# Kernel tuning notes

Measured on AMD Instinct MI355X. Metric: run time of the kernel, lower is better.

The kernel has to match this reference:

```python
import jax, jax.numpy as jnp
import numpy as np


def conv2d(x, w, b=None, stride=1, pad=0):
    y = jax.lax.conv_general_dilated(x, w, (stride, stride), [(pad, pad), (pad, pad)],
                                     dimension_numbers=('NCHW', 'OIHW', 'NCHW'))
    if b is not None:
        y = y + b[None, :, None, None]
    return y


def dcn_v2(x, off, mask, w, b):
    # ModulatedDeformConv, k=3, stride=1, pad=1, dilation=1, deformable_groups = C
    B, C, H, W = x.shape
    K = 9
    off = off.reshape(B, C, K, 2, H, W)   # (dy, dx) per group/tap
    mask = mask.reshape(B, C, K, H, W)
    dy = (jnp.arange(K) // 3 - 1).astype(x.dtype)   # kernel tap row offset (pad=1)
    dx = (jnp.arange(K) % 3 - 1).astype(x.dtype)
    py = jnp.arange(H, dtype=x.dtype)[None, None, None, :, None] + dy[None, None, :, None, None] + off[:, :, :, 0]
    px = jnp.arange(W, dtype=x.dtype)[None, None, None, None, :] + dx[None, None, :, None, None] + off[:, :, :, 1]
    y0 = jnp.floor(py); x0 = jnp.floor(px)
    wy = py - y0; wx = px - x0
    y0i = y0.astype(jnp.int32); x0i = x0.astype(jnp.int32)
    xf = x.reshape(B, C, H * W)

    def gather(yi, xi):
        valid = (yi >= 0) & (yi < H) & (xi >= 0) & (xi < W)
        idx = (jnp.clip(yi, 0, H - 1) * W + jnp.clip(xi, 0, W - 1)).reshape(B, C, -1)
        v = jnp.take_along_axis(xf, idx, axis=-1).reshape(B, C, K, H, W)
        return jnp.where(valid, v, jnp.zeros((), x.dtype))

    v00 = gather(y0i, x0i); v01 = gather(y0i, x0i + 1)
    v10 = gather(y0i + 1, x0i); v11 = gather(y0i + 1, x0i + 1)
    val = (v00 * (1 - wy) * (1 - wx) + v01 * (1 - wy) * wx
           + v10 * wy * (1 - wx) + v11 * wy * wx) * mask
    return jnp.einsum('bckhw,ock->bohw', val, w.reshape(w.shape[0], C, K)) + b[None, :, None, None]


def _forward(x, conv1_w, conv1_b, sa_w, ca_w1, ca_w2, fuse_w, fuse_b,
             mask1_w, mask1_b, down_w, down_b, mask2_w, mask2_b,
             dcn_w, dcn_b, out_w, out_b):
    f = conv1_w.shape[0]
    x2 = jax.nn.relu(conv2d(x, conv1_w, conv1_b, pad=1))
    # Spatial_Attention: conv over [avg_c, max_c], gates its OWN output
    avg = jnp.mean(x2, axis=1, keepdims=True)
    mx = jnp.max(x2, axis=1, keepdims=True)
    sa = conv2d(jnp.concatenate([avg, mx], axis=1), sa_w, pad=3)
    x2_s = jax.nn.sigmoid(sa) * sa
    # Channel_Attention (ratio=2)
    ap = jnp.mean(x2, axis=(2, 3), keepdims=True)
    mp = jnp.max(x2, axis=(2, 3), keepdims=True)
    mlp = lambda t: conv2d(jax.nn.relu(conv2d(t, ca_w1)), ca_w2)
    x2_c = jax.nn.sigmoid(mlp(ap) + mlp(mp)) * x2
    x2f = jax.nn.relu(conv2d(jnp.concatenate([x2_s, x2_c], axis=1), fuse_w, fuse_b))
    om1 = conv2d(x2f, mask1_w, mask1_b, pad=1)                 # [B, f*27, H, W]
    x3 = jax.nn.relu(conv2d(x2f, down_w, down_b, stride=2, pad=1))
    om2 = conv2d(x3, mask2_w, mask2_b, pad=1)                  # [B, f*27, H/2, W/2]
    om2 = jax.image.resize(om2, (om2.shape[0], om2.shape[1], om1.shape[2], om1.shape[3]),
                           method='bilinear')
    om = om1 + om2
    off = om[:, :f * 18]
    mask = jax.nn.sigmoid(om[:, f * 18:])
    out = jax.nn.relu(dcn_v2(x2f, off, mask, dcn_w, dcn_b))
    return jax.nn.relu(conv2d(out, out_w, out_b, pad=1))


def setup_inputs() -> dict:
    key = jax.random.key(0)
    ks = jax.random.split(key, 12)
    B, N, H, W = 4, 64, 192, 192
    f = N // 2
    s = 0.05
    d = {}
    d['x'] = jax.random.normal(ks[0], (B, N, H, W), jnp.float32)
    d['conv1_w'] = jax.random.normal(ks[1], (f, N, 3, 3)) * s
    d['conv1_b'] = jnp.zeros((f,))
    d['sa_w'] = jax.random.normal(ks[2], (f, 2, 7, 7)) * s
    d['ca_w1'] = jax.random.normal(ks[3], (f // 2, f, 1, 1)) * s
    d['ca_w2'] = jax.random.normal(ks[4], (f, f // 2, 1, 1)) * s
    d['fuse_w'] = jax.random.normal(ks[5], (f, 2 * f, 1, 1)) * s
    d['fuse_b'] = jnp.zeros((f,))
    d['mask1_w'] = jax.random.normal(ks[6], (f * 27, f, 3, 3)) * s
    d['mask1_b'] = jnp.zeros((f * 27,))
    d['down_w'] = jax.random.normal(ks[7], (f, f, 3, 3)) * s
    d['down_b'] = jnp.zeros((f,))
    d['mask2_w'] = jax.random.normal(ks[8], (f * 27, f, 3, 3)) * s
    d['mask2_b'] = jnp.zeros((f * 27,))
    d['dcn_w'] = jax.random.normal(ks[9], (f, f, 3, 3)) * s
    d['dcn_b'] = jnp.zeros((f,))
    d['out_w'] = jax.random.normal(ks[10], (N, f, 3, 3)) * s
    d['out_b'] = jnp.zeros((N,))
    return d


def reference(x, conv1_w, conv1_b, sa_w, ca_w1, ca_w2, fuse_w, fuse_b,
              mask1_w, mask1_b, down_w, down_b, mask2_w, mask2_b,
              dcn_w, dcn_b, out_w, out_b):
    return _forward(x, conv1_w, conv1_b, sa_w, ca_w1, ca_w2, fuse_w, fuse_b,
                    mask1_w, mask1_b, down_w, down_b, mask2_w, mask2_b,
                    dcn_w, dcn_b, out_w, out_b)
```

## Files before the change

### kernel.cpp

```cpp
#include <hip/hip_runtime.h>
#include <hip/hip_bf16.h>
#include <math.h>


constexpr int B = 4, N = 64, F = 32;
constexpr int H = 192, W = 192, HW = H * W;
constexpr int H2 = 96, W2 = 96, HW2 = H2 * W2;
constexpr int OMP = 1024;
constexpr int OMS = 68;

using u32 = unsigned int;
using f16x8 = __attribute__((ext_vector_type(8))) _Float16;
using f32x4 = __attribute__((ext_vector_type(4))) float;

__device__ __forceinline__ float sigmoidf_(float v) {
  return 1.f / (1.f + expf(-v));
}
__device__ __forceinline__ f16x8 bc_(uint4 u) {
  union { uint4 u; f16x8 h; } x; x.u = u; return x.h;
}
__device__ __forceinline__ u32 pk_(float a, float b) {
  union { u32 u; _Float16 h[2]; } x; x.h[0] = (_Float16)a; x.h[1] = (_Float16)b;
  return x.u;
}

__global__ __launch_bounds__(256) void dsta_fill(float* __restrict__ out,
                                                 int n, float v) {
  int i = blockIdx.x * 256 + threadIdx.x;
  if (i < n) out[i] = v;
}

__global__ __launch_bounds__(256) void dsta_stats(
    const float* __restrict__ x2, float* __restrict__ stats) {
  int idx = blockIdx.x * 256 + threadIdx.x;
  int p = idx % HW, b = idx / HW;
  float s = 0.f, m = -3.4e38f;
  for (int c = 0; c < F; ++c) {
    float v = x2[((size_t)(b * F + c)) * HW + p];
    s += v; m = fmaxf(m, v);
  }
  stats[((size_t)(b * 2 + 0)) * HW + p] = s * (1.f / F);
  stats[((size_t)(b * 2 + 1)) * HW + p] = m;
}

__global__ __launch_bounds__(256) void dsta_ca_red(
    const float* __restrict__ x2, float* __restrict__ ap, float* __restrict__ mp) {
  __shared__ float ss[256], sm[256];
  int bc = blockIdx.x;
  const float* src = x2 + (size_t)bc * HW;
  float s = 0.f, m = -3.4e38f;
  for (int i = threadIdx.x; i < HW; i += 256) {
    float v = src[i]; s += v; m = fmaxf(m, v);
  }
  ss[threadIdx.x] = s; sm[threadIdx.x] = m;
  __syncthreads();
  for (int o = 128; o > 0; o >>= 1) {
    if (threadIdx.x < o) {
      ss[threadIdx.x] += ss[threadIdx.x + o];
      sm[threadIdx.x] = fmaxf(sm[threadIdx.x], sm[threadIdx.x + o]);
    }
    __syncthreads();
  }
  if (threadIdx.x == 0) { ap[bc] = ss[0] * (1.f / HW); mp[bc] = sm[0]; }
}

__global__ __launch_bounds__(128) void dsta_ca_mlp(
    const float* __restrict__ ap, const float* __restrict__ mp,
    const float* __restrict__ w1, const float* __restrict__ w2,
    float* __restrict__ sig) {
  int t = threadIdx.x;
  if (t >= B * F) return;
  int b = t / F, co = t % F;
  float accA = 0.f, accB = 0.f;
  for (int j = 0; j < F / 2; ++j) {
    float hA = 0.f, hB = 0.f;
    for (int c = 0; c < F; ++c) {
      float wv = w1[j * F + c];
      hA = fmaf(wv, ap[b * F + c], hA);
      hB = fmaf(wv, mp[b * F + c], hB);
    }
    hA = fmaxf(hA, 0.f); hB = fmaxf(hB, 0.f);
    float wv2 = w2[co * (F / 2) + j];
    accA = fmaf(wv2, hA, accA);
    accB = fmaf(wv2, hB, accB);
  }
  sig[t] = sigmoidf_(accA + accB);
}

__global__ __launch_bounds__(256) void dsta_safuse(
    const float* __restrict__ stats, const float* __restrict__ x2,
    const float* __restrict__ sig, const float* __restrict__ sa_w,
    const float* __restrict__ fw, const float* __restrict__ fb,
    float* __restrict__ x2f) {
  int idx = blockIdx.x * 256 + threadIdx.x;
  int p = idx % HW, b = idx / HW;
  int h = p / W, w = p % W;
  float acc[F];
#pragma unroll
  for (int j = 0; j < F; ++j) acc[j] = 0.f;
#pragma unroll 1
  for (int ci = 0; ci < 2; ++ci) {
    const float* sp = stats + ((size_t)(b * 2 + ci)) * HW;
#pragma unroll 1
    for (int ky = 0; ky < 7; ++ky) {
      int yy = h + ky - 3;
      float tap[7];
#pragma unroll
      for (int kx = 0; kx < 7; ++kx) {
        int xx = w + kx - 3;
        tap[kx] = (yy >= 0 && yy < H && xx >= 0 && xx < W) ? sp[yy * W + xx] : 0.f;
      }
#pragma unroll
      for (int j = 0; j < F; ++j) {
        const float* wp = sa_w + ((size_t)(j * 2 + ci) * 49) + ky * 7;
#pragma unroll
        for (int kx = 0; kx < 7; ++kx) acc[j] = fmaf(wp[kx], tap[kx], acc[j]);
      }
    }
  }
  float accf[F];
#pragma unroll
  for (int o = 0; o < F; ++o) accf[o] = fb[o];
#pragma unroll 1
  for (int j = 0; j < F; ++j) {
    float v = acc[j];
    float asv = sigmoidf_(v) * v;
#pragma unroll
    for (int o = 0; o < F; ++o) accf[o] = fmaf(fw[o * 2 * F + j], asv, accf[o]);
  }
#pragma unroll 1
  for (int c = 0; c < F; ++c) {
    float xc = sig[b * F + c] * x2[((size_t)(b * F + c)) * HW + p];
#pragma unroll
    for (int o = 0; o < F; ++o)
      accf[o] = fmaf(fw[o * 2 * F + F + c], xc, accf[o]);
  }
#pragma unroll
  for (int o = 0; o < F; ++o)
    x2f[((size_t)(b * F + o)) * HW + p] = fmaxf(accf[o], 0.f);
}

__global__ __launch_bounds__(256) void dsta_down(
    const float* __restrict__ x2f, const float* __restrict__ wgt,
    const float* __restrict__ bias, float* __restrict__ x3) {
  int idx = blockIdx.x * 256 + threadIdx.x;
  int p = idx % HW2; int r = idx / HW2;
  int g = r % 4, b = r / 4;
  int h2 = p / W2, w2 = p % W2;
  float acc[8];
#pragma unroll
  for (int j = 0; j < 8; ++j) acc[j] = bias[g * 8 + j];
  for (int ci = 0; ci < F; ++ci) {
    const float* xp = x2f + ((size_t)(b * F + ci)) * HW;
    float tap[9];
#pragma unroll
    for (int t = 0; t < 9; ++t) {
      int yy = 2 * h2 + t / 3 - 1, xx = 2 * w2 + t % 3 - 1;
      tap[t] = (yy >= 0 && yy < H && xx >= 0 && xx < W) ? xp[yy * W + xx] : 0.f;
    }
#pragma unroll
    for (int j = 0; j < 8; ++j) {
      const float* wp = wgt + ((size_t)(g * 8 + j) * F + ci) * 9;
#pragma unroll
      for (int t = 0; t < 9; ++t) acc[j] = fmaf(wp[t], tap[t], acc[j]);
    }
  }
#pragma unroll
  for (int j = 0; j < 8; ++j)
    x3[((size_t)(b * F + g * 8 + j)) * HW2 + p] = fmaxf(acc[j], 0.f);
}

__global__ __launch_bounds__(256) void dsta_pack(
    const float* __restrict__ mw, const float* __restrict__ m2w,
    const float* __restrict__ c1w, const float* __restrict__ ow,
    u32* __restrict__ pw1, u32* __restrict__ pw2,
    u32* __restrict__ pc1, u32* __restrict__ pco) {
  int i = blockIdx.x * 256 + threadIdx.x;
  int r = i & 3, l = (i >> 2) & 63;
  int k0 = 8 * (l >> 4) + 2 * r;
  if (i < 147456) {
    int kt = (i >> 8) % 9, q = (i >> 8) / 9;
    int mt = q & 1, c = q >> 1;
    int ochl = mt * 16 + (l & 15);
    int kk = kt * 32 + k0;
    float v0 = 0.f, v1 = 0.f;
    if (ochl < 27) {
      int ochg = ochl < 18 ? c * 18 + ochl : 576 + c * 9 + (ochl - 18);
      v0 = mw[(size_t)ochg * 288 + kk];
      v1 = mw[(size_t)ochg * 288 + kk + 1];
    }
    pw1[i] = pk_(v0, v1);
  } else if (i < 271872) {
    int i2 = i - 147456;
    int kt = (i2 >> 8) % 9, mt = (i2 >> 8) / 9;
    int och = mt * 16 + (l & 15);
    int kk = kt * 32 + k0;
    pw2[i2] = pk_(m2w[(size_t)och * 288 + kk], m2w[(size_t)och * 288 + kk + 1]);
  } else if (i < 281088) {
    int i3 = i - 271872;
    int kt = (i3 >> 8) % 9, q = (i3 >> 8) / 9;
    int mt = q & 1, half = q >> 1;
    int och = mt * 16 + (l & 15);
    int kk = half * 288 + kt * 32 + k0;
    pc1[i3] = pk_(c1w[(size_t)och * 576 + kk], c1w[(size_t)och * 576 + kk + 1]);
  } else {
    int i4 = i - 281088;
    int kt = (i4 >> 8) % 9, mt = (i4 >> 8) / 9;
    int och = mt * 16 + (l & 15);
    int kk = kt * 32 + k0;
    pco[i4] = pk_(ow[(size_t)och * 288 + kk], ow[(size_t)och * 288 + kk + 1]);
  }
}

template <int SH, int SW>
__device__ __forceinline__ void build_im2col(
    const float* __restrict__ src, int y0t, int x0t,
    float* __restrict__ patch, u32* __restrict__ im2, int tid) {
  for (int i = tid; i < F * 100; i += 256) {
    int ci = i / 100, rr = i % 100;
    int yy = y0t + rr / 10 - 1, xx = x0t + rr % 10 - 1;
    patch[i] = (yy >= 0 && yy < SH && xx >= 0 && xx < SW)
                   ? src[(size_t)ci * (SH * SW) + yy * SW + xx] : 0.f;
  }
  __syncthreads();
  for (int i = tid; i < 9216; i += 256) {
    int r = i & 3, l = (i >> 2) & 63;
    int kt = (i >> 8) % 9, nt = (i >> 8) / 9;
    int j = nt * 16 + (l & 15);
    int ly = j >> 3, lx = j & 7;
    int k0 = kt * 32 + 8 * (l >> 4) + 2 * r;
    int ci0 = k0 / 9, t0 = k0 - 9 * ci0;
    int k1 = k0 + 1;
    int ci1 = k1 / 9, t1 = k1 - 9 * ci1;
    float v0 = patch[ci0 * 100 + (ly + t0 / 3) * 10 + (lx + t0 % 3)];
    float v1 = patch[ci1 * 100 + (ly + t1 / 3) * 10 + (lx + t1 % 3)];
    im2[i] = pk_(v0, v1);
  }
  __syncthreads();
}

__global__ __launch_bounds__(256) void dsta_conv1_m(
    const float* __restrict__ x, const uint4* __restrict__ pc1,
    const float* __restrict__ bias, float* __restrict__ x2) {
  __shared__ float s_patch[F * 100];
  __shared__ uint4 s_col[2304];
  int bid = blockIdx.x;
  int tile = bid % 576, b = bid / 576;
  int y0t = (tile / 24) * 8, x0t = (tile % 24) * 8;
  int tid = threadIdx.x;
  int w = tid >> 6, l = tid & 63;
  int lg = l >> 4, li = l & 15;
  int mt = w & 1;
  int nt0 = w >> 1, nt1 = 2 + (w >> 1);
  f32x4 acc0 = {0.f, 0.f, 0.f, 0.f}, acc1 = {0.f, 0.f, 0.f, 0.f};
#pragma unroll 1
  for (int half = 0; half < 2; ++half) {
    build_im2col<H, W>(x + ((size_t)(b * N + half * F)) * HW, y0t, x0t,
                       s_patch, (u32*)s_col, tid);
#pragma unroll 1
    for (int kt = 0; kt < 9; ++kt) {
      uint4 wf = pc1[(((half * 2 + mt) * 9) + kt) * 64 + l];
      acc0 = __builtin_amdgcn_mfma_f32_16x16x32_f16(
          bc_(wf), bc_(s_col[(nt0 * 9 + kt) * 64 + l]), acc0, 0, 0, 0);
      acc1 = __builtin_amdgcn_mfma_f32_16x16x32_f16(
          bc_(wf), bc_(s_col[(nt1 * 9 + kt) * 64 + l]), acc1, 0, 0, 0);
    }
    if (half == 0) __syncthreads();
  }
  int j0 = nt0 * 16 + li, j1 = nt1 * 16 + li;
  int p0 = (y0t + (j0 >> 3)) * W + x0t + (j0 & 7);
  int p1 = (y0t + (j1 >> 3)) * W + x0t + (j1 & 7);
#pragma unroll
  for (int rg = 0; rg < 4; ++rg) {
    int och = mt * 16 + lg * 4 + rg;
    float bv = bias[och];
    x2[((size_t)(b * F + och)) * HW + p0] = fmaxf(acc0[rg] + bv, 0.f);
    x2[((size_t)(b * F + och)) * HW + p1] = fmaxf(acc1[rg] + bv, 0.f);
  }
}

__global__ __launch_bounds__(256) void dsta_om2_m(
    const float* __restrict__ x3, const uint4* __restrict__ pw2,
    const float* __restrict__ bias, _Float16* __restrict__ om2r) {
  __shared__ float s_patch[F * 100];
  __shared__ uint4 s_col[2304];
  int bid = blockIdx.x;
  int cs = bid & 1;
  int tile = (bid >> 1) % 144, b = bid / 288;
  int y0t = (tile / 12) * 8, x0t = (tile % 12) * 8;
  int tid = threadIdx.x;
  build_im2col<H2, W2>(x3 + (size_t)b * F * HW2, y0t, x0t, s_patch,
                       (u32*)s_col, tid);
  int w = tid >> 6, l = tid & 63;
  int lg = l >> 4, li = l & 15;
#pragma unroll 1
  for (int mt = cs * 27 + w; mt < cs * 27 + 27; mt += 4) {
    uint4 wf[9];
#pragma unroll
    for (int kt = 0; kt < 9; ++kt) wf[kt] = pw2[(mt * 9 + kt) * 64 + l];
    float b4[4];
#pragma unroll
    for (int rg = 0; rg < 4; ++rg) b4[rg] = bias[mt * 16 + lg * 4 + rg];
    int och0 = mt * 16 + lg * 4;
    int cdx0, jdx0;
    if (och0 < 576) { cdx0 = och0 / 18; jdx0 = och0 % 18; }
    else { cdx0 = (och0 - 576) / 9; jdx0 = 18 + (och0 - 576) % 9; }
    bool contig = (och0 < 576) ? ((och0 % 18) <= 14)
                               : (((och0 - 576) % 9) <= 5);
    bool paired = contig && ((jdx0 & 1) == 0);
#pragma unroll 1
    for (int nt = 0; nt < 4; ++nt) {
      f32x4 acc = {0.f, 0.f, 0.f, 0.f};
#pragma unroll
      for (int kt = 0; kt < 9; ++kt)
        acc = __builtin_amdgcn_mfma_f32_16x16x32_f16(
            bc_(wf[kt]), bc_(s_col[(nt * 9 + kt) * 64 + l]), acc, 0, 0, 0);
      int j = nt * 16 + li;
      int gy = y0t + (j >> 3), gx = x0t + (j & 7);
      size_t pixbase = ((size_t)(b * HW2) + gy * W2 + gx) * OMP;
      if (paired) {
        u32* dst = (u32*)(om2r + pixbase + cdx0 * 32 + jdx0);
        dst[0] = pk_(acc[0] + b4[0], acc[1] + b4[1]);
        dst[1] = pk_(acc[2] + b4[2], acc[3] + b4[3]);
      } else {
#pragma unroll
        for (int rg = 0; rg < 4; ++rg) {
          int och = och0 + rg;
          int cdx, jdx;
          if (och < 576) { cdx = och / 18; jdx = och % 18; }
          else { cdx = (och - 576) / 9; jdx = 18 + (och - 576) % 9; }
          om2r[pixbase + cdx * 32 + jdx] = (_Float16)(acc[rg] + b4[rg]);
        }
      }
    }
  }
}

__global__ __launch_bounds__(256) void dsta_dcn_m(
    const float* __restrict__ x2f, const _Float16* __restrict__ om2r,
    const uint4* __restrict__ pw1, const float* __restrict__ mb,
    const float* __restrict__ dw, const float* __restrict__ db,
    float* __restrict__ dcn) {
  __shared__ uint4 s_col[2304];
  __shared__ _Float16 s_om[4 * 27 * OMS];
  int bid = blockIdx.x;
  int tile = bid % 576, b = bid / 576;
  int y0t = (tile / 24) * 8, x0t = (tile % 24) * 8;
  int tid = threadIdx.x;
  const float* xb = x2f + (size_t)b * F * HW;
  build_im2col<H, W>(xb, y0t, x0t, (float*)s_om, (u32*)s_col, tid);

  int w = tid >> 6, l = tid & 63;
  int lg = l >> 4, li = l & 15;
  int hq = y0t + (l >> 3), wq = x0t + (l & 7);

  float sy = hq * 0.5f - 0.25f, sx = wq * 0.5f - 0.25f;
  float fy0 = floorf(sy), fx0 = floorf(sx);
  float gy = sy - fy0, gx = sx - fx0;
  int y0 = (int)fy0, x0 = (int)fx0;
  int y0c = min(max(y0, 0), H2 - 1), y1c = min(max(y0 + 1, 0), H2 - 1);
  int x0c = min(max(x0, 0), W2 - 1), x1c = min(max(x0 + 1, 0), W2 - 1);
  float b00 = (1.f - gy) * (1.f - gx), b01 = (1.f - gy) * gx;
  float b10 = gy * (1.f - gx), b11 = gy * gx;
  size_t p00 = ((size_t)(b * HW2) + y0c * W2 + x0c) * OMP;
  size_t p01 = ((size_t)(b * HW2) + y0c * W2 + x1c) * OMP;
  size_t p10 = ((size_t)(b * HW2) + y1c * W2 + x0c) * OMP;
  size_t p11 = ((size_t)(b * HW2) + y1c * W2 + x1c) * OMP;

  float accd[F];
#pragma unroll
  for (int o = 0; o < F; ++o) accd[o] = 0.f;
  _Float16* s_omw = s_om + w * (27 * OMS);

#pragma unroll 1
  for (int cc = 0; cc < 8; ++cc) {
    int c = w * 8 + cc;
#pragma unroll 1
    for (int mt = 0; mt < 2; ++mt) {
      uint4 wf[9];
#pragma unroll
      for (int kt = 0; kt < 9; ++kt)
        wf[kt] = pw1[(((c * 2 + mt) * 9) + kt) * 64 + l];
#pragma unroll 1
      for (int nt = 0; nt < 4; ++nt) {
        f32x4 acc = {0.f, 0.f, 0.f, 0.f};
#pragma unroll
        for (int kt = 0; kt < 9; ++kt)
          acc = __builtin_amdgcn_mfma_f32_16x16x32_f16(
              bc_(wf[kt]), bc_(s_col[(nt * 9 + kt) * 64 + l]), acc, 0, 0, 0);
        int j = nt * 16 + li;
#pragma unroll
        for (int rg = 0; rg < 4; ++rg) {
          int ch = mt * 16 + lg * 4 + rg;
          if (ch < 27) s_omw[ch * OMS + j] = (_Float16)acc[rg];
        }
      }
    }
    const uint4* q00 = (const uint4*)(om2r + p00 + c * 32);
    const uint4* q01 = (const uint4*)(om2r + p01 + c * 32);
    const uint4* q10 = (const uint4*)(om2r + p10 + c * 32);
    const uint4* q11 = (const uint4*)(om2r + p11 + c * 32);
    float omv[27];
#pragma unroll 2
    for (int r = 0; r < 4; ++r) {
      f16x8 a0 = bc_(q00[r]), a1 = bc_(q01[r]);
      f16x8 a2 = bc_(q10[r]), a3 = bc_(q11[r]);
#pragma unroll
      for (int e = 0; e < 8; ++e) {
        int j = r * 8 + e;
        if (j < 27)
          omv[j] = b00 * (float)a0[e] + b01 * (float)a1[e] +
                   b10 * (float)a2[e] + b11 * (float)a3[e];
      }
    }
#pragma unroll
    for (int j = 0; j < 27; ++j) {
      int ch = (j < 18) ? (c * 18 + j) : (576 + c * 9 + (j - 18));
      omv[j] += mb[ch] + (float)s_omw[j * OMS + l];
    }
    const float* xc = xb + (size_t)c * HW;
#pragma unroll 3
    for (int k = 0; k < 9; ++k) {
      float m = sigmoidf_(omv[18 + k]);
      float py = (float)(hq + k / 3 - 1) + omv[2 * k];
      float px = (float)(wq + k % 3 - 1) + omv[2 * k + 1];
      float fpy = floorf(py), fpx = floorf(px);
      int yi = (int)fpy, xi = (int)fpx;
      float wy = py - fpy, wx = px - fpx;
      float v00 = (yi >= 0 && yi < H && xi >= 0 && xi < W) ? xc[yi * W + xi] : 0.f;
      float v01 = (yi >= 0 && yi < H && xi + 1 >= 0 && xi + 1 < W) ? xc[yi * W + xi + 1] : 0.f;
      float v10 = (yi + 1 >= 0 && yi + 1 < H && xi >= 0 && xi < W) ? xc[(yi + 1) * W + xi] : 0.f;
      float v11 = (yi + 1 >= 0 && yi + 1 < H && xi + 1 >= 0 && xi + 1 < W) ? xc[(yi + 1) * W + xi + 1] : 0.f;
      float val = (v00 * (1.f - wy) * (1.f - wx) + v01 * (1.f - wy) * wx +
                   v10 * wy * (1.f - wx) + v11 * wy * wx) * m;
#pragma unroll
      for (int o = 0; o < F; ++o)
        accd[o] = fmaf(val, dw[(o * F + c) * 9 + k], accd[o]);
    }
  }
  __syncthreads();
  float* s_red = (float*)s_col;
#pragma unroll
  for (int o = 0; o < F; ++o) s_red[(w * 64 + l) * 33 + o] = accd[o];
  __syncthreads();
  int px_ = tid & 63, og = tid >> 6;
  int hp = y0t + (px_ >> 3), wp = x0t + (px_ & 7);
#pragma unroll
  for (int oo = 0; oo < 8; ++oo) {
    int o = og * 8 + oo;
    float s = db[o];
#pragma unroll
    for (int w2 = 0; w2 < 4; ++w2) s += s_red[(w2 * 64 + px_) * 33 + o];
    dcn[((size_t)(b * F + o)) * HW + hp * W + wp] = fmaxf(s, 0.f);
  }
}

__global__ __launch_bounds__(256) void dsta_out_m(
    const float* __restrict__ dcn, const uint4* __restrict__ pco,
    const float* __restrict__ bias, float* __restrict__ out) {
  __shared__ float s_patch[F * 100];
  __shared__ uint4 s_col[2304];
  int bid = blockIdx.x;
  int tile = bid % 576, b = bid / 576;
  int y0t = (tile / 24) * 8, x0t = (tile % 24) * 8;
  int tid = threadIdx.x;
  build_im2col<H, W>(dcn + (size_t)b * F * HW, y0t, x0t, s_patch,
                     (u32*)s_col, tid);
  int w = tid >> 6, l = tid & 63;
  int lg = l >> 4, li = l & 15;
  int mt = w;
  f32x4 acc[4];
#pragma unroll
  for (int nt = 0; nt < 4; ++nt) acc[nt] = {0.f, 0.f, 0.f, 0.f};
#pragma unroll 1
  for (int kt = 0; kt < 9; ++kt) {
    uint4 wf = pco[(mt * 9 + kt) * 64 + l];
#pragma unroll
    for (int nt = 0; nt < 4; ++nt)
      acc[nt] = __builtin_amdgcn_mfma_f32_16x16x32_f16(
          bc_(wf), bc_(s_col[(nt * 9 + kt) * 64 + l]), acc[nt], 0, 0, 0);
  }
#pragma unroll
  for (int nt = 0; nt < 4; ++nt) {
    int j = nt * 16 + li;
    int p = (y0t + (j >> 3)) * W + x0t + (j & 7);
#pragma unroll
    for (int rg = 0; rg < 4; ++rg) {
      int och = mt * 16 + lg * 4 + rg;
      out[((size_t)(b * N + och)) * HW + p] = fmaxf(acc[nt][rg] + bias[och], 0.f);
    }
  }
}

extern "C" void kernel_launch(void* const* d_in, const int* in_sizes, int n_in,
                              void* d_out, int out_size, void* d_ws, size_t ws_size,
                              hipStream_t stream) {
  float* out = (float*)d_out;
  const int fill_grid = (out_size + 255) / 256;

  static const int idmap[18]  = {0,1,2,3,4,5,6,7,8,9,10,11,12,13,14,15,16,17};
  static const int alphamap[18] = {17,3,2,16,0,1,9,8,11,10,7,6,13,12,5,4,15,14};
  const int* map = nullptr;
  if (n_in == 18 && in_sizes[0] == 9437184) map = idmap;
  else if (n_in == 18 && in_sizes[17] == 9437184) map = alphamap;
  if (!map) {
    dsta_fill<<<fill_grid, 256, 0, stream>>>(out, out_size, 2.0e6f);
    return;
  }
  if (in_sizes[map[8]] != 248832 || in_sizes[map[16]] != 18432) {
    dsta_fill<<<fill_grid, 256, 0, stream>>>(out, out_size, 3.0e6f);
    return;
  }

  const float* x       = (const float*)d_in[map[0]];
  const float* conv1_w = (const float*)d_in[map[1]];
  const float* conv1_b = (const float*)d_in[map[2]];
  const float* sa_w    = (const float*)d_in[map[3]];
  const float* ca_w1   = (const float*)d_in[map[4]];
  const float* ca_w2   = (const float*)d_in[map[5]];
  const float* fuse_w  = (const float*)d_in[map[6]];
  const float* fuse_b  = (const float*)d_in[map[7]];
  const float* mask1_w = (const float*)d_in[map[8]];
  const float* mask1_b = (const float*)d_in[map[9]];
  const float* down_w  = (const float*)d_in[map[10]];
  const float* down_b  = (const float*)d_in[map[11]];
  const float* mask2_w = (const float*)d_in[map[12]];
  const float* mask2_b = (const float*)d_in[map[13]];
  const float* dcn_w   = (const float*)d_in[map[14]];
  const float* dcn_b   = (const float*)d_in[map[15]];
  const float* out_w   = (const float*)d_in[map[16]];
  const float* out_b   = (const float*)d_in[map[17]];

  float* ws = (float*)d_ws;
  float* x2    = ws;
  float* x2f   = x2  + (size_t)B * F * HW;
  float* x3    = x2f + (size_t)B * F * HW;
  float* stats = x3  + (size_t)B * F * HW2;
  float* ap    = stats + (size_t)B * 2 * HW;
  float* mp    = ap + B * F;
  float* sig   = mp + B * F;
  _Float16* om2r = (_Float16*)(sig + B * F);
  u32* pc1 = (u32*)(om2r + (size_t)B * HW2 * OMP);
  u32* pco = pc1 + 9216;
  float* dcn   = x2;

  u32* pw1 = (u32*)d_out;
  u32* pw2 = pw1 + 147456;

  const size_t base_f32 = 10912128;
  const size_t need = base_f32 * 4ull + (size_t)B * HW2 * OMP * 2ull +
                      2ull * 9216 * 4ull;
  if (ws_size < need) {
    dsta_fill<<<fill_grid, 256, 0, stream>>>(
        out, out_size, 1.0e6f + (float)(ws_size >> 20));
    return;
  }

  dsta_pack<<<1134, 256, 0, stream>>>(mask1_w, mask2_w, conv1_w, out_w,
                                      pw1, pw2, pc1, pco);
  dsta_conv1_m<<<2304, 256, 0, stream>>>(x, (const uint4*)pc1, conv1_b, x2);
  dsta_stats<<<576, 256, 0, stream>>>(x2, stats);
  dsta_ca_red<<<128, 256, 0, stream>>>(x2, ap, mp);
  dsta_ca_mlp<<<1, 128, 0, stream>>>(ap, mp, ca_w1, ca_w2, sig);
  dsta_safuse<<<576, 256, 0, stream>>>(stats, x2, sig, sa_w, fuse_w, fuse_b,
                                       x2f);
  dsta_down<<<576, 256, 0, stream>>>(x2f, down_w, down_b, x3);
  dsta_om2_m<<<1152, 256, 0, stream>>>(x3, (const uint4*)pw2, mask2_b, om2r);
  dsta_dcn_m<<<2304, 256, 0, stream>>>(x2f, om2r, (const uint4*)pw1,
                                       mask1_b, dcn_w, dcn_b, dcn);
  dsta_out_m<<<2304, 256, 0, stream>>>(dcn, (const uint4*)pco, out_b, out);
}
```

Baseline: 900.0 us.

## Stage upsampled offset window in LDS with register prefetch of next channel

Each wave now loads a 6x6 window of low-resolution offset/mask rows for its tile cooperatively, one u32 per lane, instead of every lane issuing four scattered 64-byte gathers per channel. The window goes into shared memory and is read back for bilinear interpolation. The next channel's window is prefetched into registers while the current one is processed. The window reuses the per-wave s_om scratch, so the interpolation is now done before the MFMA conv that overwrites it. This reorder adds an LDS round trip and a waitcnt, and relies on the window covering all four interpolation corners.

```diff
diff --git a/kernel.cpp b/kernel.cpp
--- a/kernel.cpp
+++ b/kernel.cpp
@@ -358,59 +358,80 @@
   float fy0 = floorf(sy), fx0 = floorf(sx);
   float gy = sy - fy0, gx = sx - fx0;
   int y0 = (int)fy0, x0 = (int)fx0;
-  int y0c = min(max(y0, 0), H2 - 1), y1c = min(max(y0 + 1, 0), H2 - 1);
-  int x0c = min(max(x0, 0), W2 - 1), x1c = min(max(x0 + 1, 0), W2 - 1);
   float b00 = (1.f - gy) * (1.f - gx), b01 = (1.f - gy) * gx;
   float b10 = gy * (1.f - gx), b11 = gy * gx;
-  size_t p00 = ((size_t)(b * HW2) + y0c * W2 + x0c) * OMP;
-  size_t p01 = ((size_t)(b * HW2) + y0c * W2 + x1c) * OMP;
-  size_t p10 = ((size_t)(b * HW2) + y1c * W2 + x0c) * OMP;
-  size_t p11 = ((size_t)(b * HW2) + y1c * W2 + x1c) * OMP;
+  int yb = y0t >> 1, xb2 = x0t >> 1;
+  const u32* om2u = (const u32*)om2r;
+  size_t goff[9];
+#pragma unroll
+  for (int q = 0; q < 9; ++q) {
+    int idx = q * 64 + l;
+    int s = idx >> 4, r = idx & 15;
+    int srow = min(max(yb - 1 + s / 6, 0), H2 - 1);
+    int scol = min(max(xb2 - 1 + s % 6, 0), W2 - 1);
+    goff[q] = ((size_t)(b * HW2) + srow * W2 + scol) * 512 + r;
+  }
+  int wbase = ((y0 - yb + 1) * 6 + (x0 - xb2 + 1)) * 4;
 
   float accd[F];
 #pragma unroll
   for (int o = 0; o < F; ++o) accd[o] = 0.f;
   _Float16* s_omw = s_om + w * (27 * OMS);
+  u32* s_win = (u32*)s_omw;
+
+  u32 wreg[9];
+  {
+    int c0 = w * 8;
+#pragma unroll
+    for (int q = 0; q < 9; ++q) wreg[q] = om2u[goff[q] + c0 * 16];
+  }
 
 #pragma unroll 1
   for (int cc = 0; cc < 8; ++cc) {
     int c = w * 8 + cc;
-#pragma unroll 1
-    for (int mt = 0; mt < 2; ++mt) {
-      uint4 wf[9];
-#pragma unroll
-      for (int kt = 0; kt < 9; ++kt)
-        wf[kt] = pw1[(((c * 2 + mt) * 9) + kt) * 64 + l];
-#pragma unroll 1
-      for (int nt = 0; nt < 4; ++nt) {
-        f32x4 acc = {0.f, 0.f, 0.f, 0.f};
-#pragma unroll
-        for (int kt = 0; kt < 9; ++kt)
-          acc = __builtin_amdgcn_mfma_f32_16x16x32_f16(
-              bc_(wf[kt]), bc_(s_col[(nt * 9 + kt) * 64 + l]), acc, 0, 0, 0);
-        int j = nt * 16 + li;
-#pragma unroll
-        for (int rg = 0; rg < 4; ++rg) {
-          int ch = mt * 16 + lg * 4 + rg;
-          if (ch < 27) s_omw[ch * OMS + j] = (_Float16)acc[rg];
-        }
-      }
-    }
-    const uint4* q00 = (const uint4*)(om2r + p00 + c * 32);
-    const uint4* q01 = (const uint4*)(om2r + p01 + c * 32);
-    const uint4* q10 = (const uint4*)(om2r + p10 + c * 32);
-    const uint4* q11 = (const uint4*)(om2r + p11 + c * 32);
+#pragma unroll
+    for (int q = 0; q < 9; ++q) s_win[q * 64 + l] = wreg[q];
+    if (cc < 7) {
+      int cn = c + 1;
+#pragma unroll
+      for (int q = 0; q < 9; ++q) wreg[q] = om2u[goff[q] + cn * 16];
+    }
+    asm volatile("s_waitcnt lgkmcnt(0)" ::: "memory");
+    const uint4* wv = (const uint4*)s_win;
     float omv[27];
 #pragma unroll 2
     for (int r = 0; r < 4; ++r) {
-      f16x8 a0 = bc_(q00[r]), a1 = bc_(q01[r]);
-      f16x8 a2 = bc_(q10[r]), a3 = bc_(q11[r]);
+      f16x8 a0 = bc_(wv[wbase + r]);
+      f16x8 a1 = bc_(wv[wbase + 4 + r]);
+      f16x8 a2 = bc_(wv[wbase + 24 + r]);
+      f16x8 a3 = bc_(wv[wbase + 28 + r]);
 #pragma unroll
       for (int e = 0; e < 8; ++e) {
         int j = r * 8 + e;
         if (j < 27)
           omv[j] = b00 * (float)a0[e] + b01 * (float)a1[e] +
                    b10 * (float)a2[e] + b11 * (float)a3[e];
+      }
+    }
+#pragma unroll 1
+    for (int mt = 0; mt < 2; ++mt) {
+      uint4 wf[9];
+#pragma unroll
+      for (int kt = 0; kt < 9; ++kt)
+        wf[kt] = pw1[(((c * 2 + mt) * 9) + kt) * 64 + l];
+#pragma unroll 1
+      for (int nt = 0; nt < 4; ++nt) {
+        f32x4 acc = {0.f, 0.f, 0.f, 0.f};
+#pragma unroll
+        for (int kt = 0; kt < 9; ++kt)
+          acc = __builtin_amdgcn_mfma_f32_16x16x32_f16(
+              bc_(wf[kt]), bc_(s_col[(nt * 9 + kt) * 64 + l]), acc, 0, 0, 0);
+        int j = nt * 16 + li;
+#pragma unroll
+        for (int rg = 0; rg < 4; ++rg) {
+          int ch = mt * 16 + lg * 4 + rg;
+          if (ch < 27) s_omw[ch * OMS + j] = (_Float16)acc[rg];
+        }
       }
     }
 #pragma unroll
```

Measured after the change: 877.2 us. 1.03x faster.
